# Optimization experiments

Measured on AMD Instinct MI355X. Metric: run time of the kernel, lower is better.

## Reference

```python
import jax, jax.numpy as jnp
import numpy as np

N, E, F_DIM = 30000, 480000, 256
CLS_HID, NUM_CLASS, GEN_HID, MI_HID, BATCH = 128, 16, 64, 128, 4096
COM_L1, COM_L2, LAM, ALPHA, TAU, EPS = 0.5, 0.5, 0.5, 1.0, 0.5, 1e-8


def _glorot(key, shape):
    scale = jnp.sqrt(2.0 / (shape[0] + shape[-1]))
    return scale * jax.random.normal(key, shape, dtype=jnp.float32)


def setup_inputs() -> dict:
    key = jax.random.key(0)
    ks = jax.random.split(key, 32)
    inp = {
        'feat': jax.random.normal(ks[0], (N, F_DIM), dtype=jnp.float32),
        'view1_indices': jax.random.randint(ks[1], (2, E), 0, N),
        'view1_values': jax.random.uniform(ks[2], (E,), dtype=jnp.float32),
        'view2_indices': jax.random.randint(ks[3], (2, E), 0, N),
        'view2_values': jax.random.uniform(ks[4], (E,), dtype=jnp.float32),
        'idx': jnp.sort(jax.random.randint(ks[5], (BATCH,), 0, N)),
        # GenView (v1 and v2): gen_gcn weight + gen_mlp (Linear(2*gen_hid, 1))
        'W_gen_v1': _glorot(ks[6], (F_DIM, GEN_HID)),
        'Wm_v1': _glorot(ks[7], (2 * GEN_HID, 1)),
        'bm_v1': jnp.zeros((1,), dtype=jnp.float32),
        'W_gen_v2': _glorot(ks[8], (F_DIM, GEN_HID)),
        'Wm_v2': _glorot(ks[9], (2 * GEN_HID, 1)),
        'bm_v2': jnp.zeros((1,), dtype=jnp.float32),
        # Classification: three two-layer GCN encoders (v1, v2, v)
        'W1_v1': _glorot(ks[10], (F_DIM, CLS_HID)), 'W2_v1': _glorot(ks[11], (CLS_HID, NUM_CLASS)),
        'W1_v2': _glorot(ks[12], (F_DIM, CLS_HID)), 'W2_v2': _glorot(ks[13], (CLS_HID, NUM_CLASS)),
        'W1_v': _glorot(ks[14], (F_DIM, CLS_HID)), 'W2_v': _glorot(ks[15], (CLS_HID, NUM_CLASS)),
        # MI_NCE: three single GCN layers + shared projection MLP
        'Wg': _glorot(ks[16], (F_DIM, MI_HID)),
        'Wg1': _glorot(ks[17], (F_DIM, MI_HID)),
        'Wg2': _glorot(ks[18], (F_DIM, MI_HID)),
        'Wp1': _glorot(ks[19], (MI_HID, MI_HID)), 'bp1': jnp.zeros((MI_HID,), dtype=jnp.float32),
        'Wp2': _glorot(ks[20], (MI_HID, MI_HID)), 'bp2': jnp.zeros((MI_HID,), dtype=jnp.float32),
    }
    return inp


def spmm(idx, vals, x, n):
    # sparse COO adj (idx [2,E], vals [E]) @ dense x [n,d]
    return jax.ops.segment_sum(vals[:, None] * x[idx[1]], idx[0], num_segments=n)


def gcn_layer(x, idx, vals, W, n, act):
    h = spmm(idx, vals, x @ W, n)
    return jax.nn.relu(h) if act else h


def two_layer(x, idx, vals, W1, W2, n):
    return gcn_layer(gcn_layer(x, idx, vals, W1, n, True), idx, vals, W2, n, False)


def sparse_row_softmax(scores, rows, n):
    m = jax.lax.stop_gradient(jax.ops.segment_max(scores, rows, num_segments=n))
    e = jnp.exp(scores - m[rows])
    s = jax.ops.segment_sum(e, rows, num_segments=n)
    return e / s[rows]


def gen_view(feat, idx, vals, Wg, Wm, bm, com_lambda, n):
    emb = gcn_layer(feat, idx, vals, Wg, n, True)
    ff = jnp.concatenate([emb[idx[0]], emb[idx[1]]], axis=-1)  # [E, 2*gen_hid]
    temp = (ff @ Wm + bm).reshape(-1)
    pi = sparse_row_softmax(temp, idx[0], n)  # torch.sparse.softmax(dim=1)
    return vals + com_lambda * pi  # same sparsity pattern as v_ori


def sym(idx, vals):
    # normalize1 (big=True): adj + adj.T as COO concat (duplicates sum in spmm)
    return jnp.concatenate([idx, idx[::-1]], axis=1), jnp.concatenate([vals, vals])


def get_weight(prob):
    top2 = jax.lax.top_k(prob, 2)[0]
    fir, sec = top2[:, 0], top2[:, 1]
    return jnp.exp(ALPHA * (LAM * jnp.log(fir + EPS) + (1.0 - LAM) * jnp.log(fir - sec + EPS)))


def contrast_cal(z1, z2):
    num = z1 @ z2.T
    den = jnp.linalg.norm(z1, axis=-1, keepdims=True) @ jnp.linalg.norm(z2, axis=-1, keepdims=True).T
    m12 = jnp.exp(num / den / TAU)
    m21 = m12.T
    l12 = -jnp.log(jnp.diag(m12 / (m12.sum(1, keepdims=True) + EPS)) + EPS).mean()
    l21 = -jnp.log(jnp.diag(m21 / (m21.sum(1, keepdims=True) + EPS)) + EPS).mean()
    return 0.5 * (l12 + l21)


def cogsl_forward(feat, view1_values, view2_values,
                  W_gen_v1, Wm_v1, bm_v1, W_gen_v2, Wm_v2, bm_v2,
                  W1_v1, W2_v1, W1_v2, W2_v2, W1_v, W2_v,
                  Wg, Wg1, Wg2, Wp1, bp1, Wp2, bp2,
                  view1_indices, view2_indices, idx):
    n = feat.shape[0]
    # View_Estimator (GenView + normalize1)
    nv1 = gen_view(feat, view1_indices, view1_values, W_gen_v1, Wm_v1, bm_v1, COM_L1, n)
    nv2 = gen_view(feat, view2_indices, view2_values, W_gen_v2, Wm_v2, bm_v2, COM_L2, n)
    i1, v1 = sym(view1_indices, nv1)
    i2, v2 = sym(view2_indices, nv2)
    # Classification on each generated view
    prob_v1 = jax.nn.softmax(two_layer(feat, i1, v1, W1_v1, W2_v1, n), axis=1)
    prob_v2 = jax.nn.softmax(two_layer(feat, i2, v2, W1_v2, W2_v2, n), axis=1)
    logits_v1 = jnp.log(prob_v1 + EPS)
    logits_v2 = jnp.log(prob_v2 + EPS)
    # Fusion: per-node convex combination of the two sparse views (row scaling)
    w1 = get_weight(prob_v1)
    w2 = get_weight(prob_v2)
    b1 = w1 / (w1 + w2)
    b2 = w2 / (w1 + w2)
    idx_f = jnp.concatenate([i1, i2], axis=1)
    vals_f = jnp.concatenate([b1[i1[0]] * v1, b2[i2[0]] * v2])
    prob_v = jax.nn.softmax(two_layer(feat, idx_f, vals_f, W1_v, W2_v, n), axis=1)
    logits_v = jnp.log(prob_v + EPS)
    # MI_NCE over [fused v, v1, v2], big=True -> sample `batch` nodes
    proj = lambda h: jax.nn.elu(h @ Wp1 + bp1) @ Wp2 + bp2
    ev = proj(gcn_layer(feat, idx_f, vals_f, Wg, n, True))[idx]
    e1 = proj(gcn_layer(feat, i1, v1, Wg1, n, True))[idx]
    e2 = proj(gcn_layer(feat, i2, v2, Wg2, n, True))[idx]
    vv1 = contrast_cal(ev, e1)
    vv2 = contrast_cal(ev, e2)
    v1v2 = contrast_cal(e1, e2)
    return jnp.concatenate([logits_v.ravel(), logits_v1.ravel(), logits_v2.ravel(),
                            jnp.stack([vv1, vv2, v1v2])])


def reference(feat, view1_indices, view1_values, view2_indices, view2_values, idx,
              W_gen_v1, Wm_v1, bm_v1, W_gen_v2, Wm_v2, bm_v2,
              W1_v1, W2_v1, W1_v2, W2_v2, W1_v, W2_v,
              Wg, Wg1, Wg2, Wp1, bp1, Wp2, bp2):
    return cogsl_forward(feat, view1_values, view2_values,
                         W_gen_v1, Wm_v1, bm_v1, W_gen_v2, Wm_v2, bm_v2,
                         W1_v1, W2_v1, W1_v2, W2_v2, W1_v, W2_v,
                         Wg, Wg1, Wg2, Wp1, bp1, Wp2, bp2,
                         view1_indices, view2_indices, idx)
```

## Files before the change

### kernel.cpp

```cpp
#include <hip/hip_runtime.h>
#include <math.h>

#define NN 30000
#define EE 480000
#define FD 256
#define CH 128
#define NCLS 16
#define GH 64
#define MH 128
#define BT 4096
#define EPSc 1e-8f
#define GBc ((NN + 127) / 128)
#define SPB8 ((NN + 7) / 8)
#define SPB16 ((NN + 15) / 16)
#define RBc ((BT + 15) / 16)
#define NOX (SPB16 + 3 * RBc)

typedef __attribute__((ext_vector_type(8))) short short8;
typedef __attribute__((ext_vector_type(4))) float f32x4;

__device__ __forceinline__ unsigned short f2bf(float x) {
    unsigned b = __float_as_uint(x);
    unsigned r = b + 0x7FFFu + ((b >> 16) & 1u);
    return (unsigned short)(r >> 16);
}
__device__ __forceinline__ float bf2f(unsigned short h) {
    return __uint_as_float(((unsigned)h) << 16);
}
__device__ __forceinline__ float4 fma4(float s, float4 x, float4 a) {
    a.x = fmaf(s, x.x, a.x); a.y = fmaf(s, x.y, a.y);
    a.z = fmaf(s, x.z, a.z); a.w = fmaf(s, x.w, a.w);
    return a;
}

__global__ void split_bf16(const float* __restrict__ x, unsigned short* __restrict__ hi,
                           unsigned short* __restrict__ lo, long n) {
    long i = (long)blockIdx.x * 256 + threadIdx.x;
    if (i >= n) return;
    float v = x[i];
    unsigned short h = f2bf(v);
    hi[i] = h;
    lo[i] = f2bf(v - bf2f(h));
}

struct WSArgs {
    const float* s[8];
    unsigned short* h[8];
    unsigned short* l[8];
};
__global__ void wsplit_all(WSArgs a) {
    constexpr int NNp[8] = {64, 64, 128, 128, 128, 128, 128, 128};
    constexpr int OFF[9] = {0, 16384, 32768, 65536, 98304, 131072, 163840, 196608, 229376};
    int i = blockIdx.x * 256 + threadIdx.x;
    if (i >= 229376) return;
    int w = 0;
#pragma unroll
    for (int t = 1; t < 8; t++) if (i >= OFF[t]) w = t;
    int j = i - OFF[w];
    int N = NNp[w];
    int k = j / N, n = j % N;
    float v = a.s[w][j];
    unsigned short hh = f2bf(v);
    a.h[w][(size_t)n * 256 + k] = hh;
    a.l[w][(size_t)n * 256 + k] = f2bf(v - bf2f(hh));
}

template <int NT, bool OUT16>
__device__ __forceinline__ void gemm3_body(
    unsigned short* sm, int bx,
    const unsigned short* __restrict__ Ahi, const unsigned short* __restrict__ Alo,
    const unsigned short* __restrict__ BThi, const unsigned short* __restrict__ BTlo,
    int K, void* __restrict__ Cv, int Cstride, int M)
{
    unsigned short* Ah = sm;
    unsigned short* Al = Ah + 128 * 40;
    unsigned short* Bh = Al + 128 * 40;
    unsigned short* Bl = Bh + NT * 16 * 40;
    int t = threadIdx.x;
    int w = t >> 6, l = t & 63;
    int lane = l & 15, quad = l >> 4;
    int row0 = bx * 128;
    f32x4 acc[2][NT];
#pragma unroll
    for (int s = 0; s < 2; s++)
#pragma unroll
        for (int n = 0; n < NT; n++) acc[s][n] = (f32x4)(0.f);

    int ar = t >> 1, ako = (t & 1) << 4;
    int nkc = K >> 5;
    for (int kc = 0; kc < nkc; kc++) {
        int kb = kc << 5;
        {
            int gr = row0 + ar;
            float4 h0, h1, l0, l1;
            if (gr < M) {
                const float4* pH = (const float4*)&Ahi[(size_t)gr * K + kb + ako];
                const float4* pL = (const float4*)&Alo[(size_t)gr * K + kb + ako];
                h0 = pH[0]; h1 = pH[1]; l0 = pL[0]; l1 = pL[1];
            } else {
                h0 = h1 = l0 = l1 = make_float4(0.f, 0.f, 0.f, 0.f);
            }
            float4* dH = (float4*)&Ah[ar * 40 + ako];
            dH[0] = h0; dH[1] = h1;
            float4* dL = (float4*)&Al[ar * 40 + ako];
            dL[0] = l0; dL[1] = l1;
        }
        if (ar < NT * 16) {
            const float4* pH = (const float4*)&BThi[(size_t)ar * K + kb + ako];
            const float4* pL = (const float4*)&BTlo[(size_t)ar * K + kb + ako];
            float4 h0 = pH[0], h1 = pH[1], l0 = pL[0], l1 = pL[1];
            float4* dH = (float4*)&Bh[ar * 40 + ako];
            dH[0] = h0; dH[1] = h1;
            float4* dL = (float4*)&Bl[ar * 40 + ako];
            dL[0] = l0; dL[1] = l1;
        }
        __syncthreads();
        short8 aH[2], aL[2];
// ... 58 lines not shown
    int nkc = K >> 5;
    for (int kc = 0; kc < nkc; kc++) {
        int kb = kc << 5;
        {
            int gr = row0 + ar;
            float4 h0, h1;
            if (gr < M) {
                const float4* pH = (const float4*)&Ahi[(size_t)gr * K + kb + ako];
                h0 = pH[0]; h1 = pH[1];
            } else {
                h0 = h1 = make_float4(0.f, 0.f, 0.f, 0.f);
            }
            float4* dH = (float4*)&Ah[ar * 40 + ako];
            dH[0] = h0; dH[1] = h1;
        }
        if (ar < NT * 16) {
            const float4* pH = (const float4*)&BThi[(size_t)ar * K + kb + ako];
            float4 h0 = pH[0], h1 = pH[1];
            float4* dH = (float4*)&Bh[ar * 40 + ako];
            dH[0] = h0; dH[1] = h1;
        }
        __syncthreads();
        short8 aH[2];
#pragma unroll
        for (int s = 0; s < 2; s++)
            aH[s] = *(const short8*)&Ah[(w * 32 + s * 16 + lane) * 40 + quad * 8];
#pragma unroll
        for (int n = 0; n < NT; n++) {
            short8 bH = *(const short8*)&Bh[(n * 16 + lane) * 40 + quad * 8];
#pragma unroll
            for (int s = 0; s < 2; s++)
                acc[s][n] = __builtin_amdgcn_mfma_f32_16x16x32_bf16(aH[s], bH, acc[s][n], 0, 0, 0);
        }
        __syncthreads();
    }
#pragma unroll
    for (int s = 0; s < 2; s++) {
        int rb = row0 + w * 32 + s * 16 + quad * 4;
#pragma unroll
        for (int reg = 0; reg < 4; reg++) {
            int gr = rb + reg;
            if (gr >= M) continue;
#pragma unroll
            for (int n = 0; n < NT; n++) {
                if (OUT16)
                    ((unsigned short*)Cv)[(size_t)gr * Cstride + n * 16 + lane] = f2bf(acc[s][n][reg]);
                else
                    ((float*)Cv)[(size_t)gr * Cstride + n * 16 + lane] = acc[s][n][reg];
            }
        }
    }
}

__global__ __launch_bounds__(256) void mega0(
    const int* __restrict__ i1, const int* __restrict__ i2, int* __restrict__ cnt,
    int* __restrict__ sd1, int* __restrict__ sd2,
    int* __restrict__ sc1, int* __restrict__ sc2,
    const unsigned short* __restrict__ feat_hi,
    const unsigned short* __restrict__ w1vh, unsigned short* __restrict__ Ph2,
    const unsigned short* __restrict__ wgallh, unsigned short* __restrict__ Pmi16)
{
    __shared__ unsigned short sm[128 * 40 + 8 * 16 * 40];
    int b = blockIdx.x;
    if (b < GBc) {
        gemm1_body<8, true>(sm, b, feat_hi, w1vh, FD, Ph2, 128, NN);
        return;
    }
    b -= GBc;
    if (b < 3 * GBc) {
        int y = b / GBc, bx = b % GBc;
        gemm1_body<8, true>(sm, bx, feat_hi, wgallh + (size_t)y * 32768,
                            FD, Pmi16 + (size_t)y * 128, 384, NN);
        return;
    }
    b -= 3 * GBc;
    int e = b * 256 + threadIdx.x;
    if (e >= EE) return;
    int r1 = i1[e], c1 = i1[EE + e];
    int r2 = i2[e], c2 = i2[EE + e];
    sd1[e] = atomicAdd(&cnt[r1], 1);
    sd2[e] = atomicAdd(&cnt[NN + r2], 1);
    sc1[e] = atomicAdd(&cnt[2 * NN + c1], 1);
    sc2[e] = atomicAdd(&cnt[3 * NN + c2], 1);
}

__global__ __launch_bounds__(256) void mega1(
    const int* __restrict__ i1, const float* __restrict__ v1,
    const int* __restrict__ i2, const float* __restrict__ v2,
    const int* __restrict__ sd1, const int* __restrict__ sd2,
    const int* __restrict__ sc1, const int* __restrict__ sc2,
    const int* __restrict__ rp4,
    int2* __restrict__ ed1, int2* __restrict__ ec1,
    int2* __restrict__ ed2, int2* __restrict__ ec2,
    const unsigned short* __restrict__ feat_hi, const unsigned short* __restrict__ feat_lo,
    const unsigned short* __restrict__ wgen12h, const unsigned short* __restrict__ wgen12l,
    float* __restrict__ Pg,
    const unsigned short* __restrict__ w1pairh, const unsigned short* __restrict__ w1pairl,
    float* __restrict__ P01)
{
    __shared__ unsigned short sm[128 * 40 * 2 + 8 * 16 * 40 * 2];
    int b = blockIdx.x;
    if (b < GBc) {
        gemm3_body<8, false>(sm, b, feat_hi, feat_lo, wgen12h, wgen12l, FD, Pg, 128, NN);
        return;
    }
    b -= GBc;
    if (b < 2 * GBc) {
        int y = b / GBc, bx = b % GBc;
        gemm3_body<8, false>(sm, bx, feat_hi, feat_lo,
                             w1pairh + (size_t)y * 32768, w1pairl + (size_t)y * 32768,
                             FD, P01 + (size_t)y * 128, 256, NN);
        return;
    }
    b -= 2 * GBc;
    int e = b * 256 + threadIdx.x;
    if (e >= EE) return;
    const int* rp_d1 = rp4;
    const int* rp_d2 = rp4 + (NN + 1);
    const int* rp_c1 = rp4 + 2 * (NN + 1);
    const int* rp_c2 = rp4 + 3 * (NN + 1);
    int r = i1[e], c = i1[EE + e];
    int p = rp_d1[r] + sd1[e];
    ed1[p] = make_int2(c, __float_as_int(v1[e]));
    ec1[rp_c1[c] + sc1[e]] = make_int2(r, p);
    r = i2[e]; c = i2[EE + e];
    p = rp_d2[r] + sd2[e];
    ed2[p] = make_int2(c, __float_as_int(v2[e]));
    ec2[rp_c2[c] + sc2[e]] = make_int2(r, p);
}

__global__ __launch_bounds__(256) void contrast_direct(
    const unsigned short* __restrict__ z16, float* __restrict__ stats)
{
    int p = blockIdx.z;
    int pa = (p == 2) ? 1 : 0;
    int pb = (p == 0) ? 1 : 2;
    const unsigned short* A = z16 + (size_t)pa * BT * MH;
    const unsigned short* B = z16 + (size_t)pb * BT * MH;
    float* diag = stats + (size_t)p * 3 * BT;
    float* rs = diag + BT;
    float* cs = rs + BT;
    int t = threadIdx.x;
    int w = t >> 6, l = t & 63, m = l & 15, quad = l >> 4;
    int i0 = blockIdx.y * 128, j0 = blockIdx.x * 128;

    short8 afr[2][4];
#pragma unroll
    for (int s = 0; s < 2; s++) {
        const unsigned short* arow = &A[(size_t)(i0 + w * 32 + s * 16 + m) * MH + quad * 8];
#pragma unroll
        for (int kc = 0; kc < 4; kc++)
            afr[s][kc] = *(const short8*)(arow + kc * 32);
    }
    f32x4 acc[2][8];
#pragma unroll
    for (int s = 0; s < 2; s++)
#pragma unroll
        for (int n = 0; n < 8; n++) acc[s][n] = (f32x4)(0.f);

#pragma unroll
    for (int kc = 0; kc < 4; kc++) {
#pragma unroll
        for (int n = 0; n < 8; n++) {
            short8 bf = *(const short8*)&B[(size_t)(j0 + n * 16 + m) * MH + kc * 32 + quad * 8];
            acc[0][n] = __builtin_amdgcn_mfma_f32_16x16x32_bf16(afr[0][kc], bf, acc[0][n], 0, 0, 0);
            acc[1][n] = __builtin_amdgcn_mfma_f32_16x16x32_bf16(afr[1][kc], bf, acc[1][n], 0, 0, 0);
        }
// ... 192 lines not shown
    const int* rp = rp_d + y * (NN + 1);
    const int2* arr = y ? e2 : e1;
    int row = blockIdx.x * 16 + threadIdx.x / 16;
    int o = threadIdx.x % 16;
    if (row >= NN) return;
    float4 a[4] = {};
    gath_dir_f32<32>(rp, arr, row, (const float4*)Pg, y * 16 + o, a);
    float4 r;
    r.x = fmaxf((a[0].x + a[1].x) + (a[2].x + a[3].x), 0.f);
    r.y = fmaxf((a[0].y + a[1].y) + (a[2].y + a[3].y), 0.f);
    r.z = fmaxf((a[0].z + a[1].z) + (a[2].z + a[3].z), 0.f);
    r.w = fmaxf((a[0].w + a[1].w) + (a[2].w + a[3].w), 0.f);
    const float* Wmh = (y ? Wm2 : Wm1) + GH;
    float part = r.x * Wmh[o * 4] + r.y * Wmh[o * 4 + 1]
               + r.z * Wmh[o * 4 + 2] + r.w * Wmh[o * 4 + 3];
    part += __shfl_xor(part, 1); part += __shfl_xor(part, 2);
    part += __shfl_xor(part, 4); part += __shfl_xor(part, 8);
    if (o == 0) sb[y * NN + row] = part;
}

__device__ __forceinline__ void softmax16_epi(
    float4 r, int node, float* __restrict__ logits, float* __restrict__ wout)
{
    int o = threadIdx.x & 3;
    float mx = fmaxf(fmaxf(r.x, r.y), fmaxf(r.z, r.w));
    mx = fmaxf(mx, __shfl_xor(mx, 1));
    mx = fmaxf(mx, __shfl_xor(mx, 2));
    float e0 = expf(r.x - mx), e1 = expf(r.y - mx), e2 = expf(r.z - mx), e3 = expf(r.w - mx);
    float s = (e0 + e1) + (e2 + e3);
    s += __shfl_xor(s, 1);
    s += __shfl_xor(s, 2);
    float inv = 1.f / s;
    float p0 = e0 * inv, p1 = e1 * inv, p2 = e2 * inv, p3 = e3 * inv;
    float4 lg;
    lg.x = logf(p0 + EPSc); lg.y = logf(p1 + EPSc);
    lg.z = logf(p2 + EPSc); lg.w = logf(p3 + EPSc);
    ((float4*)logits)[(size_t)node * 4 + o] = lg;
    if (wout) {
        float f = p0, se = -1.f;
        if (p1 > f) { se = f; f = p1; } else se = p1;
        if (p2 > f) { se = f; f = p2; } else if (p2 > se) se = p2;
        if (p3 > f) { se = f; f = p3; } else if (p3 > se) se = p3;
#pragma unroll
        for (int d = 1; d <= 2; d <<= 1) {
            float of = __shfl_xor(f, d), os = __shfl_xor(se, d);
            if (of > f) { se = fmaxf(f, os); f = of; }
            else se = fmaxf(se, of);
        }
        if (o == 0)
            wout[node] = expf(0.5f * logf(f + EPSc) + 0.5f * logf(f - se + EPSc));
    }
}

__global__ __launch_bounds__(256) void spmm16_softmax_pair(
    const int* __restrict__ rp_d, const int* __restrict__ rp_c,
    const int2* __restrict__ ed1, const int2* __restrict__ ec1, const float* __restrict__ nvd1,
    const int2* __restrict__ ed2, const int2* __restrict__ ec2, const float* __restrict__ nvd2,
    const float* __restrict__ R01, float* __restrict__ logits_base, float* __restrict__ w12)
{
    int y = blockIdx.y;
    const int* rpd = rp_d + y * (NN + 1);
    const int* rpc = rp_c + y * (NN + 1);
    const int2* ed = y ? ed2 : ed1;
    const int2* ec = y ? ec2 : ec1;
    const float* nvd = y ? nvd2 : nvd1;
    int row = blockIdx.x * 64 + threadIdx.x / 4;
    int o = threadIdx.x % 4;
    if (row >= NN) return;
    const float4* x4 = (const float4*)(R01 + (size_t)y * NN * 16);
    float4 a[4] = {};
    gath_dir_f32<4>(rpd, ed, row, x4, o, a);
    gath_csc_f32<4>(rpc, ec, nvd, row, x4, o, a);
    float4 r;
    r.x = (a[0].x + a[1].x) + (a[2].x + a[3].x);
    r.y = (a[0].y + a[1].y) + (a[2].y + a[3].y);
    r.z = (a[0].z + a[1].z) + (a[2].z + a[3].z);
    r.w = (a[0].w + a[1].w) + (a[2].w + a[3].w);
    softmax16_epi(r, row, logits_base + (size_t)y * NN * NCLS, w12 + (size_t)y * NN);
}

__global__ __launch_bounds__(256) void spmm16_fused_softmax(
    const int* __restrict__ rp_d, const int* __restrict__ rp_c,
    const int2* __restrict__ ed1, const int2* __restrict__ ec1, const float* __restrict__ nvd1,
    const int2* __restrict__ ed2, const int2* __restrict__ ec2, const float* __restrict__ nvd2,
    const float* __restrict__ w12, const float* __restrict__ x, float* __restrict__ logits)
{
    int row = blockIdx.x * 64 + threadIdx.x / 4;
    int o = threadIdx.x % 4;
    if (row >= NN) return;
    const float4* x4 = (const float4*)x;
    float4 a[4] = {};
    gath_dir_f32<4>(rp_d, ed1, row, x4, o, a);
    gath_csc_f32<4>(rp_c, ec1, nvd1, row, x4, o, a);
    float4 s1;
    s1.x = (a[0].x + a[1].x) + (a[2].x + a[3].x);
    s1.y = (a[0].y + a[1].y) + (a[2].y + a[3].y);
    s1.z = (a[0].z + a[1].z) + (a[2].z + a[3].z);
    s1.w = (a[0].w + a[1].w) + (a[2].w + a[3].w);
    float4 b[4] = {};
    gath_dir_f32<4>(rp_d + (NN + 1), ed2, row, x4, o, b);
    gath_csc_f32<4>(rp_c + (NN + 1), ec2, nvd2, row, x4, o, b);
    float4 s2;
    s2.x = (b[0].x + b[1].x) + (b[2].x + b[3].x);
    s2.y = (b[0].y + b[1].y) + (b[2].y + b[3].y);
    s2.z = (b[0].z + b[1].z) + (b[2].z + b[3].z);
    s2.w = (b[0].w + b[1].w) + (b[2].w + b[3].w);
    float wa = w12[row], wb = w12[NN + row];
    float inv = 1.f / (wa + wb);
    float w1 = wa * inv, w2 = wb * inv;
    float4 r;
    r.x = w1 * s1.x + w2 * s2.x;
    r.y = w1 * s1.y + w2 * s2.y;
    r.z = w1 * s1.z + w2 * s2.z;
    r.w = w1 * s1.w + w2 * s2.w;
    softmax16_epi(r, row, logits, nullptr);
}

__device__ __forceinline__ void gath_dir_b16(
    const int* __restrict__ rp, const int2* __restrict__ ed, int row,
    const unsigned short* __restrict__ X, int xstride, int o, float* acc)
{
    int p0 = rp[row], p1 = rp[row + 1];
    int j = p0;
    for (; j + 8 <= p1; j += 8) {
        int2 q[8]; short8 x[8];
#pragma unroll
        for (int e = 0; e < 8; e++) q[e] = ed[j + e];
#pragma unroll
        for (int e = 0; e < 8; e++)
            x[e] = *(const short8*)&X[(size_t)q[e].x * xstride + o * 8];
#pragma unroll
        for (int e = 0; e < 8; e++) {
            float v = __int_as_float(q[e].y);
#pragma unroll
            for (int k = 0; k < 8; k++)
                acc[k] = fmaf(v, bf2f((unsigned short)x[e][k]), acc[k]);
        }
    }
    for (; j + 4 <= p1; j += 4) {
        int2 q0 = ed[j], q1 = ed[j+1], q2 = ed[j+2], q3 = ed[j+3];
// ... 130 lines not shown
    int row = bx * 16 + r;
    if (row >= NN) return;
    float a1[8] = {}, a2[8] = {};
    gath_dir_b16(rp_d, ed1, row, Ph2, 128, o, a1);
    gath_csc_b16(rp_c, ec1, nvd1, row, Ph2, 128, o, a1);
    gath_dir_b16(rp_d + (NN + 1), ed2, row, Ph2, 128, o, a2);
    gath_csc_b16(rp_c + (NN + 1), ec2, nvd2, row, Ph2, 128, o, a2);
    float* o1 = A1 + (size_t)row * 128 + o * 8;
    float* o2 = A2 + (size_t)row * 128 + o * 8;
    *(float4*)&o1[0] = make_float4(a1[0], a1[1], a1[2], a1[3]);
    *(float4*)&o1[4] = make_float4(a1[4], a1[5], a1[6], a1[7]);
    *(float4*)&o2[0] = make_float4(a2[0], a2[1], a2[2], a2[3]);
    *(float4*)&o2[4] = make_float4(a2[4], a2[5], a2[6], a2[7]);
}

__device__ __forceinline__ void spmm128f_body(
    float* sm, int bx, int y, const int* __restrict__ rp_d, const int* __restrict__ rp_c,
    const int2* __restrict__ ed, const int2* __restrict__ ec, const float* __restrict__ nvd,
    const float* __restrict__ P01, const float* __restrict__ W2, float* __restrict__ R01)
{
    float* W2s = sm;
    float* Qs  = sm + 2048;
    for (int i = threadIdx.x; i < 2048; i += 256) W2s[i] = W2[i];
    int r = threadIdx.x / 32;
    int o = threadIdx.x % 32;
    int row = bx * 8 + r;
    float4 a[4] = {};
    if (row < NN) {
        gath_dir_f32<64>(rp_d + y * (NN + 1), ed, row, (const float4*)P01, y * 32 + o, a);
        gath_csc_f32<64>(rp_c + y * (NN + 1), ec, nvd, row, (const float4*)P01, y * 32 + o, a);
    }
    float4 q;
    q.x = fmaxf((a[0].x + a[1].x) + (a[2].x + a[3].x), 0.f);
    q.y = fmaxf((a[0].y + a[1].y) + (a[2].y + a[3].y), 0.f);
    q.z = fmaxf((a[0].z + a[1].z) + (a[2].z + a[3].z), 0.f);
    q.w = fmaxf((a[0].w + a[1].w) + (a[2].w + a[3].w), 0.f);
    *(float4*)&Qs[r * 128 + o * 4] = q;
    __syncthreads();
    int t = threadIdx.x;
    if (t < 128) {
        int rr = t >> 4, c = t & 15;
        int grow = bx * 8 + rr;
        if (grow < NN) {
            float acc = 0.f;
            const float* qrow = &Qs[rr * 128];
#pragma unroll 8
            for (int k = 0; k < 128; k++)
                acc = fmaf(qrow[k], W2s[k * 16 + c], acc);
            R01[((size_t)y * NN + grow) * 16 + c] = acc;
        }
    }
}

__global__ __launch_bounds__(256) void mega23(
    const int* __restrict__ rp_d, const int* __restrict__ rp_c,
    const int2* __restrict__ ed1, const int2* __restrict__ ec1, const float* __restrict__ nvd1,
    const int2* __restrict__ ed2, const int2* __restrict__ ec2, const float* __restrict__ nvd2,
    const float* __restrict__ P01, const float* __restrict__ W2v1, const float* __restrict__ W2v2,
    float* __restrict__ R01,
    const int* __restrict__ rows, const unsigned short* __restrict__ Pmi,
    float* __restrict__ zQ,
    const unsigned short* __restrict__ Ph2,
    float* __restrict__ A1, float* __restrict__ A2,
    float* __restrict__ G1, float* __restrict__ G2)
{
    __shared__ float sm[2048 + 8 * 128];
    int b = blockIdx.x;
    int u = b >> 2, r = b & 3;
    if (r == 3) {
        if (u < SPB16) {
            b2gather_body(u, rp_d, rp_c, ed1, ec1, nvd1, ed2, ec2, nvd2, Ph2, A1, A2);
            return;
        }
        u -= SPB16;
        if (u < 2 * RBc) {
            int y = 1 + u / RBc;
            rows_b16_body(u % RBc, y, rp_d, rp_c, ed1, ec1, nvd1, ed2, ec2, nvd2,
                          rows, Pmi, zQ);
            return;
        }
        u -= 2 * RBc;
        rows0_gather_body(u, rp_d, rp_c, ed1, ec1, nvd1, ed2, ec2, nvd2,
                          rows, Pmi, G1, G2);
        return;
    }
    int s = u * 3 + r;
    if (s >= 2 * SPB8) return;
    int y = s / SPB8;
    spmm128f_body(sm, s % SPB8, y, rp_d, rp_c, y ? ed2 : ed1, y ? ec2 : ec1,
                  y ? nvd2 : nvd1, P01, y ? W2v2 : W2v1, R01);
}

__global__ __launch_bounds__(256) void combineB2(
    const float* __restrict__ w12,
    const float* __restrict__ A1, const float* __restrict__ A2,
    const float* __restrict__ W2v, float* __restrict__ R2,
    const int* __restrict__ rows,
    const float* __restrict__ G1, const float* __restrict__ G2,
    float* __restrict__ zQ)
{
    __shared__ float sm[2048 + 16 * 128];
    int b = blockIdx.x;
    int r = threadIdx.x / 16;
    int o = threadIdx.x % 16;
    if (b < SPB16) {
        float* W2s = sm;
        float* Qs  = sm + 2048;
        for (int i = threadIdx.x; i < 2048; i += 256) W2s[i] = W2v[i];
        int row = b * 16 + r;
        float wa = w12[row], wb = w12[NN + row];
        float inv = 1.f / (wa + wb);
        float w1 = wa * inv, w2 = wb * inv;
        const float* p1 = A1 + (size_t)row * 128 + o * 8;
        const float* p2 = A2 + (size_t)row * 128 + o * 8;
#pragma unroll
        for (int k = 0; k < 8; k++)
            Qs[r * 128 + o * 8 + k] = fmaxf(w1 * p1[k] + w2 * p2[k], 0.f);
        __syncthreads();
        int t = threadIdx.x;
        int rr = t >> 4, c = t & 15;
        int grow = b * 16 + rr;
        float acc = 0.f;
        const float* qrow = &Qs[rr * 128];
#pragma unroll 8
        for (int k = 0; k < 128; k++)
            acc = fmaf(qrow[k], W2s[k * 16 + c], acc);
        R2[(size_t)grow * 16 + c] = acc;
        return;
    }
    b -= SPB16;
    int ri = b * 16 + r;
    if (ri >= BT) return;
    int node = rows[ri];
    float wa = w12[node], wb = w12[NN + node];
    float inv = 1.f / (wa + wb);
    float w1 = wa * inv, w2 = wb * inv;
    const float* p1 = G1 + (size_t)ri * 128 + o * 8;
    const float* p2 = G2 + (size_t)ri * 128 + o * 8;
    float* out = zQ + (size_t)ri * 128 + o * 8;
#pragma unroll
    for (int k = 0; k < 8; k++)
        out[k] = fmaxf(w1 * p1[k] + w2 * p2[k], 0.f);
}

__global__ __launch_bounds__(256) void proj_norm8(
    const float* __restrict__ zQ,
    const float* __restrict__ Wp1, const float* __restrict__ bp1,
    const float* __restrict__ Wp2, const float* __restrict__ bp2,
    unsigned short* __restrict__ z16)
{
    __shared__ float g[8 * MH], u[8 * MH];
    __shared__ float red[4][4];
    int t = threadIdx.x;
    size_t base = (size_t)blockIdx.y * BT + (size_t)blockIdx.x * 8;
    for (int idx = t; idx < 8 * MH; idx += 256)
        g[idx] = zQ[(base + (idx >> 7)) * MH + (idx & 127)];
    __syncthreads();
    int col = t & 127;
    int rh = t >> 7;
    float acc[4];
    float b1 = bp1[col];
#pragma unroll
    for (int rr = 0; rr < 4; rr++) acc[rr] = b1;
    for (int k = 0; k < MH; k++) {
        float wk = Wp1[k * MH + col];
#pragma unroll
        for (int rr = 0; rr < 4; rr++)
            acc[rr] = fmaf(g[(rh * 4 + rr) * MH + k], wk, acc[rr]);
    }
#pragma unroll
    for (int rr = 0; rr < 4; rr++)
        u[(rh * 4 + rr) * MH + col] = acc[rr] > 0.f ? acc[rr] : (expf(acc[rr]) - 1.f);
    __syncthreads();
    float z[4];
    float b2 = bp2[col];
#pragma unroll
    for (int rr = 0; rr < 4; rr++) z[rr] = b2;
    for (int k = 0; k < MH; k++) {
        float wk = Wp2[k * MH + col];
#pragma unroll
        for (int rr = 0; rr < 4; rr++)
            z[rr] = fmaf(u[(rh * 4 + rr) * MH + k], wk, z[rr]);
    }
    float sq[4];
#pragma unroll
    for (int rr = 0; rr < 4; rr++) sq[rr] = z[rr] * z[rr];
#pragma unroll
    for (int off = 32; off; off >>= 1) {
#pragma unroll
        for (int rr = 0; rr < 4; rr++) sq[rr] += __shfl_xor(sq[rr], off);
    }
    int w = t >> 6;
    if ((t & 63) == 0) {
#pragma unroll
        for (int rr = 0; rr < 4; rr++) red[w][rr] = sq[rr];
    }
    __syncthreads();
#pragma unroll
    for (int rr = 0; rr < 4; rr++) {
        float nrm = sqrtf(red[rh * 2][rr] + red[rh * 2 + 1][rr]);
        z16[(base + rh * 4 + rr) * MH + col] = f2bf(z[rr] / nrm);
    }
}

__global__ void contrast_reduce(const float* __restrict__ stats, float* __restrict__ out3)
{
    int p = blockIdx.x, t = threadIdx.x;
    const float* diag = stats + (size_t)p * 3 * BT;
    const float* rs = diag + BT;
    const float* cs = rs + BT;
    float s1 = 0.f, s2 = 0.f;
    for (int i = t; i < BT; i += 256) {
        float d = diag[i];
        s1 += logf(d / (rs[i] + EPSc) + EPSc);
        s2 += logf(d / (cs[i] + EPSc) + EPSc);
    }
#pragma unroll
    for (int off = 32; off; off >>= 1) { s1 += __shfl_down(s1, off); s2 += __shfl_down(s2, off); }
    __shared__ float sh[8];
    if ((t & 63) == 0) { sh[(t >> 6) * 2] = s1; sh[(t >> 6) * 2 + 1] = s2; }
    __syncthreads();
    if (t == 0) {
        float a = sh[0] + sh[2] + sh[4] + sh[6];
        float b = sh[1] + sh[3] + sh[5] + sh[7];
        out3[p] = 0.5f * (-a / BT - b / BT);
    }
}

extern "C" void kernel_launch(void* const* d_in, const int* in_sizes, int n_in,
                              void* d_out, int out_size, void* d_ws, size_t ws_size,
                              hipStream_t stream)
{
    const float* feat   = (const float*)d_in[0];
    const int*   ind1   = (const int*)d_in[1];
    const float* vals1  = (const float*)d_in[2];
    const int*   ind2   = (const int*)d_in[3];
    const float* vals2  = (const float*)d_in[4];
    const int*   idxb   = (const int*)d_in[5];
    const float* Wm1    = (const float*)d_in[7];
    const float* Wm2    = (const float*)d_in[10];
    const float* W2_v1  = (const float*)d_in[13];
    const float* W2_v2  = (const float*)d_in[15];
    const float* W2_v   = (const float*)d_in[17];
    const float* Wp1    = (const float*)d_in[21];
    const float* bp1    = (const float*)d_in[22];
    const float* Wp2    = (const float*)d_in[23];
    const float* bp2    = (const float*)d_in[24];
    float* dout = (float*)d_out;

    float* ws = (float*)d_ws;
    size_t off = 0;
    auto alloc = [&](size_t n) { n = (n + 3) & ~(size_t)3; float* p = ws + off; off += n; return p; };
    auto alloc_s = [&](size_t n) { return (unsigned short*)alloc((n + 1) / 2); };

    float* pool = alloc(16000000);
    float* Pg   = pool;
    float* P01  = pool + 3840000;
    float* R01  = pool + 11520000;
    float* zQ   = pool + 12480000;
    float* A1   = pool;
    float* G1   = pool + 14052864;
    float* G2   = pool + 14577152;
    float* R2   = pool + 15101440;

    unsigned short* feat_hi = alloc_s((size_t)NN * FD);
    unsigned short* feat_lo = alloc_s((size_t)NN * FD);
    float* A2 = (float*)feat_hi;
    unsigned short* Ph2d    = alloc_s((size_t)NN * CH);
    unsigned short* Pmi16d  = alloc_s((size_t)NN * 384);
    float* sb   = alloc(2 * NN);
    float* w12  = alloc(2 * NN);
    float* stats = alloc((size_t)3 * 3 * BT);
    unsigned short* z16 = alloc_s((size_t)3 * BT * MH);
    int2* ed1 = (int2*)alloc(2 * (size_t)EE);
    int2* ed2 = (int2*)alloc(2 * (size_t)EE);
    int2* ec1 = (int2*)alloc(2 * (size_t)EE);
    int2* ec2 = (int2*)alloc(2 * (size_t)EE);
    float* nvd1 = alloc(EE);
    float* nvd2 = alloc(EE);
    int* sd1 = (int*)alloc(EE);
    int* sd2 = (int*)alloc(EE);
    int* sc1 = (int*)alloc(EE);
    int* sc2 = (int*)alloc(EE);
    int* rp4  = (int*)alloc(4 * (NN + 1));
    int* cnt4 = (int*)alloc(4 * NN);
    int* bsum = (int*)alloc(128);
    int* rp_d = rp4;
    int* rp_c = rp4 + 2 * (NN + 1);
    unsigned short* wgen12h = alloc_s(32768); unsigned short* wgen12l = alloc_s(32768);
    unsigned short* w1pairh = alloc_s(65536); unsigned short* w1pairl = alloc_s(65536);
    unsigned short* w1vh    = alloc_s(32768); unsigned short* w1vl    = alloc_s(32768);
    unsigned short* wgallh  = alloc_s(98304); unsigned short* wgalll  = alloc_s(98304);

    const int NB = (NN + 1 + 1023) / 1024;
    const int NCNT = (EE + 255) / 256;

    hipMemsetAsync(cnt4, 0, 4 * NN * 4, stream);
    split_bf16<<<((long)NN * FD + 255) / 256, 256, 0, stream>>>(feat, feat_hi, feat_lo, (long)NN * FD);
    {
        WSArgs a;
        a.s[0] = (const float*)d_in[6];  a.h[0] = wgen12h;          a.l[0] = wgen12l;
        a.s[1] = (const float*)d_in[9];  a.h[1] = wgen12h + 16384;  a.l[1] = wgen12l + 16384;
        a.s[2] = (const float*)d_in[12]; a.h[2] = w1pairh;          a.l[2] = w1pairl;
        a.s[3] = (const float*)d_in[14]; a.h[3] = w1pairh + 32768;  a.l[3] = w1pairl + 32768;
        a.s[4] = (const float*)d_in[16]; a.h[4] = w1vh;             a.l[4] = w1vl;
        a.s[5] = (const float*)d_in[18]; a.h[5] = wgallh;           a.l[5] = wgalll;
        a.s[6] = (const float*)d_in[19]; a.h[6] = wgallh + 32768;   a.l[6] = wgalll + 32768;
        a.s[7] = (const float*)d_in[20]; a.h[7] = wgallh + 65536;   a.l[7] = wgalll + 65536;
        wsplit_all<<<(229376 + 255) / 256, 256, 0, stream>>>(a);
    }

    mega0<<<4 * GBc + NCNT, 256, 0, stream>>>(ind1, ind2, cnt4, sd1, sd2, sc1, sc2,
                                              feat_hi, w1vh, Ph2d, wgallh, Pmi16d);

    scan_block4<<<dim3(NB, 4), 1024, 0, stream>>>(cnt4, rp4, bsum);
    scan_bsum4<<<4, 64, 0, stream>>>(bsum, NB);
    scan_add4<<<dim3(NB, 4), 1024, 0, stream>>>(bsum, rp4);

    mega1<<<3 * GBc + NCNT, 256, 0, stream>>>(ind1, vals1, ind2, vals2,
                                              sd1, sd2, sc1, sc2, rp4,
                                              ed1, ec1, ed2, ec2,
                                              feat_hi, feat_lo, wgen12h, wgen12l, Pg,
                                              w1pairh, w1pairl, P01);

    spmm64_scores<<<dim3((NN + 15) / 16, 2), 256, 0, stream>>>(rp_d, ed1, ed2, Pg, Wm1, Wm2, sb);
    gen_nv<<<dim3((NN + 255) / 256, 2), 256, 0, stream>>>(rp_d, ed1, ed2, sb, nvd1, nvd2);

    mega23<<<4 * NOX, 256, 0, stream>>>(rp_d, rp_c, ed1, ec1, nvd1,
                                        ed2, ec2, nvd2, P01, W2_v1, W2_v2,
                                        R01, idxb, Pmi16d, zQ,
                                        Ph2d, A1, A2, G1, G2);

    spmm16_softmax_pair<<<dim3((NN + 63) / 64, 2), 256, 0, stream>>>(
        rp_d, rp_c, ed1, ec1, nvd1, ed2, ec2, nvd2, R01, dout + (size_t)NN * NCLS, w12);

    combineB2<<<SPB16 + RBc, 256, 0, stream>>>(w12, A1, A2, W2_v, R2, idxb, G1, G2, zQ);

    spmm16_fused_softmax<<<(NN + 63) / 64, 256, 0, stream>>>(
        rp_d, rp_c, ed1, ec1, nvd1, ed2, ec2, nvd2, w12, R2, dout);

    proj_norm8<<<dim3(BT / 8, 3), 256, 0, stream>>>(zQ, Wp1, bp1, Wp2, bp2, z16);
    hipMemsetAsync(stats, 0, (size_t)3 * 3 * BT * 4, stream);
    contrast_direct<<<dim3(32, 32, 3), 256, 0, stream>>>(z16, stats);
    contrast_reduce<<<3, 256, 0, stream>>>(stats, dout + (size_t)3 * NN * NCLS);
}
```

Baseline: 883.3 us.

## Regroup kernel launches into fewer mega-kernels by dependency stage

Merges the feature split, weight split and edge counting into one prep kernel, and moves the bf16 GEMMs for Ph2 and Pmi into mega1x. The old mega23 is split so spmm128f and the rows_b16 gathers run first (mega2). The pair softmax then runs alongside the b2/rows0 gathers and the projection of planes 1 and 2 (pairX), and the plane-0 projection runs alongside the fused softmax (fusedX). The aim is to cut launch count and idle tails by overlapping independent work in each launch, at the cost of more heterogeneous blocks and possible imbalance, such as the GEMMs now sharing a launch with scatter work.

```diff
diff --git a/kernel.cpp b/kernel.cpp
--- a/kernel.cpp
+++ b/kernel.cpp
@@ -14,7 +14,9 @@
 #define SPB8 ((NN + 7) / 8)
 #define SPB16 ((NN + 15) / 16)
 #define RBc ((BT + 15) / 16)
-#define NOX (SPB16 + 3 * RBc)
+#define PRB ((NN + 63) / 64)
+#define PJB (BT / 8)
+#define PX4 1056
 
 typedef __attribute__((ext_vector_type(8))) short short8;
 typedef __attribute__((ext_vector_type(4))) float f32x4;
@@ -31,16 +33,6 @@
     a.x = fmaf(s, x.x, a.x); a.y = fmaf(s, x.y, a.y);
     a.z = fmaf(s, x.z, a.z); a.w = fmaf(s, x.w, a.w);
     return a;
-}
-
-__global__ void split_bf16(const float* __restrict__ x, unsigned short* __restrict__ hi,
-                           unsigned short* __restrict__ lo, long n) {
-    long i = (long)blockIdx.x * 256 + threadIdx.x;
-    if (i >= n) return;
-    float v = x[i];
-    unsigned short h = f2bf(v);
-    hi[i] = h;
-    lo[i] = f2bf(v - bf2f(h));
 }
 
 struct WSArgs {
@@ -48,21 +40,50 @@
     unsigned short* h[8];
     unsigned short* l[8];
 };
-__global__ void wsplit_all(WSArgs a) {
-    constexpr int NNp[8] = {64, 64, 128, 128, 128, 128, 128, 128};
-    constexpr int OFF[9] = {0, 16384, 32768, 65536, 98304, 131072, 163840, 196608, 229376};
-    int i = blockIdx.x * 256 + threadIdx.x;
-    if (i >= 229376) return;
-    int w = 0;
-#pragma unroll
-    for (int t = 1; t < 8; t++) if (i >= OFF[t]) w = t;
-    int j = i - OFF[w];
-    int N = NNp[w];
-    int k = j / N, n = j % N;
-    float v = a.s[w][j];
-    unsigned short hh = f2bf(v);
-    a.h[w][(size_t)n * 256 + k] = hh;
-    a.l[w][(size_t)n * 256 + k] = f2bf(v - bf2f(hh));
+
+__global__ __launch_bounds__(256) void prep_all(
+    const float* __restrict__ feat, unsigned short* __restrict__ fhi,
+    unsigned short* __restrict__ flo, WSArgs a,
+    const int* __restrict__ i1, const int* __restrict__ i2, int* __restrict__ cnt,
+    int* __restrict__ sd1, int* __restrict__ sd2,
+    int* __restrict__ sc1, int* __restrict__ sc2)
+{
+    int b = blockIdx.x;
+    if (b < 30000) {
+        long i = (long)b * 256 + threadIdx.x;
+        float v = feat[i];
+        unsigned short h = f2bf(v);
+        fhi[i] = h;
+        flo[i] = f2bf(v - bf2f(h));
+        return;
+    }
+    b -= 30000;
+    if (b < 896) {
+        int i = b * 256 + threadIdx.x;
+        if (i >= 229376) return;
+        constexpr int NNp[8] = {64, 64, 128, 128, 128, 128, 128, 128};
+        constexpr int OFF[9] = {0, 16384, 32768, 65536, 98304, 131072, 163840, 196608, 229376};
+        int w = 0;
+#pragma unroll
+        for (int t = 1; t < 8; t++) if (i >= OFF[t]) w = t;
+        int j = i - OFF[w];
+        int N = NNp[w];
+        int k = j / N, n = j % N;
+        float v = a.s[w][j];
+        unsigned short hh = f2bf(v);
+        a.h[w][(size_t)n * 256 + k] = hh;
+        a.l[w][(size_t)n * 256 + k] = f2bf(v - bf2f(hh));
+        return;
+    }
+    b -= 896;
+    int e = b * 256 + threadIdx.x;
+    if (e >= EE) return;
+    int r1 = i1[e], c1 = i1[EE + e];
+    int r2 = i2[e], c2 = i2[EE + e];
+    sd1[e] = atomicAdd(&cnt[r1], 1);
+    sd2[e] = atomicAdd(&cnt[NN + r2], 1);
+    sc1[e] = atomicAdd(&cnt[2 * NN + c1], 1);
+    sc2[e] = atomicAdd(&cnt[3 * NN + c2], 1);
 }
 
 template <int NT, bool OUT16>
@@ -227,39 +248,7 @@
     }
 }
 
-__global__ __launch_bounds__(256) void mega0(
-    const int* __restrict__ i1, const int* __restrict__ i2, int* __restrict__ cnt,
-    int* __restrict__ sd1, int* __restrict__ sd2,
-    int* __restrict__ sc1, int* __restrict__ sc2,
-    const unsigned short* __restrict__ feat_hi,
-    const unsigned short* __restrict__ w1vh, unsigned short* __restrict__ Ph2,
-    const unsigned short* __restrict__ wgallh, unsigned short* __restrict__ Pmi16)
-{
-    __shared__ unsigned short sm[128 * 40 + 8 * 16 * 40];
-    int b = blockIdx.x;
-    if (b < GBc) {
-        gemm1_body<8, true>(sm, b, feat_hi, w1vh, FD, Ph2, 128, NN);
-        return;
-    }
-    b -= GBc;
-    if (b < 3 * GBc) {
-        int y = b / GBc, bx = b % GBc;
-        gemm1_body<8, true>(sm, bx, feat_hi, wgallh + (size_t)y * 32768,
-                            FD, Pmi16 + (size_t)y * 128, 384, NN);
-        return;
-    }
-    b -= 3 * GBc;
-    int e = b * 256 + threadIdx.x;
-    if (e >= EE) return;
-    int r1 = i1[e], c1 = i1[EE + e];
-    int r2 = i2[e], c2 = i2[EE + e];
-    sd1[e] = atomicAdd(&cnt[r1], 1);
-    sd2[e] = atomicAdd(&cnt[NN + r2], 1);
-    sc1[e] = atomicAdd(&cnt[2 * NN + c1], 1);
-    sc2[e] = atomicAdd(&cnt[3 * NN + c2], 1);
-}
-
-__global__ __launch_bounds__(256) void mega1(
+__global__ __launch_bounds__(256) void mega1x(
     const int* __restrict__ i1, const float* __restrict__ v1,
     const int* __restrict__ i2, const float* __restrict__ v2,
     const int* __restrict__ sd1, const int* __restrict__ sd2,
@@ -271,7 +260,9 @@
     const unsigned short* __restrict__ wgen12h, const unsigned short* __restrict__ wgen12l,
     float* __restrict__ Pg,
     const unsigned short* __restrict__ w1pairh, const unsigned short* __restrict__ w1pairl,
-    float* __restrict__ P01)
+    float* __restrict__ P01,
+    const unsigned short* __restrict__ w1vh, unsigned short* __restrict__ Ph2,
+    const unsigned short* __restrict__ wgallh, unsigned short* __restrict__ Pmi16)
 {
     __shared__ unsigned short sm[128 * 40 * 2 + 8 * 16 * 40 * 2];
     int b = blockIdx.x;
@@ -288,6 +279,18 @@
         return;
     }
     b -= 2 * GBc;
+    if (b < GBc) {
+        gemm1_body<8, true>(sm, b, feat_hi, w1vh, FD, Ph2, 128, NN);
+        return;
+    }
+    b -= GBc;
+    if (b < 3 * GBc) {
+        int y = b / GBc, bx = b % GBc;
+        gemm1_body<8, true>(sm, bx, feat_hi, wgallh + (size_t)y * 32768,
+                            FD, Pmi16 + (size_t)y * 128, 384, NN);
+        return;
+    }
+    b -= 3 * GBc;
     int e = b * 256 + threadIdx.x;
     if (e >= EE) return;
     const int* rp_d1 = rp4;
@@ -586,19 +589,18 @@
     }
 }
 
-__global__ __launch_bounds__(256) void spmm16_softmax_pair(
-    const int* __restrict__ rp_d, const int* __restrict__ rp_c,
+__device__ __forceinline__ void pair_body(
+    int y, int bx, const int* __restrict__ rp_d, const int* __restrict__ rp_c,
     const int2* __restrict__ ed1, const int2* __restrict__ ec1, const float* __restrict__ nvd1,
     const int2* __restrict__ ed2, const int2* __restrict__ ec2, const float* __restrict__ nvd2,
     const float* __restrict__ R01, float* __restrict__ logits_base, float* __restrict__ w12)
 {
-    int y = blockIdx.y;
     const int* rpd = rp_d + y * (NN + 1);
     const int* rpc = rp_c + y * (NN + 1);
     const int2* ed = y ? ed2 : ed1;
     const int2* ec = y ? ec2 : ec1;
     const float* nvd = y ? nvd2 : nvd1;
-    int row = blockIdx.x * 64 + threadIdx.x / 4;
+    int row = bx * 64 + threadIdx.x / 4;
     int o = threadIdx.x % 4;
     if (row >= NN) return;
     const float4* x4 = (const float4*)(R01 + (size_t)y * NN * 16);
@@ -613,13 +615,13 @@
     softmax16_epi(r, row, logits_base + (size_t)y * NN * NCLS, w12 + (size_t)y * NN);
 }
 
-__global__ __launch_bounds__(256) void spmm16_fused_softmax(
-    const int* __restrict__ rp_d, const int* __restrict__ rp_c,
+__device__ __forceinline__ void fused_body(
+    int bx, const int* __restrict__ rp_d, const int* __restrict__ rp_c,
     const int2* __restrict__ ed1, const int2* __restrict__ ec1, const float* __restrict__ nvd1,
     const int2* __restrict__ ed2, const int2* __restrict__ ec2, const float* __restrict__ nvd2,
     const float* __restrict__ w12, const float* __restrict__ x, float* __restrict__ logits)
 {
-    int row = blockIdx.x * 64 + threadIdx.x / 4;
+    int row = bx * 64 + threadIdx.x / 4;
     int o = threadIdx.x % 4;
     if (row >= NN) return;
     const float4* x4 = (const float4*)x;
@@ -856,43 +858,127 @@
     }
 }
 
-__global__ __launch_bounds__(256) void mega23(
+__global__ __launch_bounds__(256) void mega2(
     const int* __restrict__ rp_d, const int* __restrict__ rp_c,
     const int2* __restrict__ ed1, const int2* __restrict__ ec1, const float* __restrict__ nvd1,
     const int2* __restrict__ ed2, const int2* __restrict__ ec2, const float* __restrict__ nvd2,
     const float* __restrict__ P01, const float* __restrict__ W2v1, const float* __restrict__ W2v2,
     float* __restrict__ R01,
     const int* __restrict__ rows, const unsigned short* __restrict__ Pmi,
-    float* __restrict__ zQ,
-    const unsigned short* __restrict__ Ph2,
-    float* __restrict__ A1, float* __restrict__ A2,
-    float* __restrict__ G1, float* __restrict__ G2)
+    float* __restrict__ zQ)
 {
     __shared__ float sm[2048 + 8 * 128];
     int b = blockIdx.x;
+    if (b < 2 * SPB8) {
+        int y = b / SPB8;
+        spmm128f_body(sm, b % SPB8, y, rp_d, rp_c, y ? ed2 : ed1, y ? ec2 : ec1,
+                      y ? nvd2 : nvd1, P01, y ? W2v2 : W2v1, R01);
+        return;
+    }
+    b -= 2 * SPB8;
+    int y = 1 + b / RBc;
+    rows_b16_body(b % RBc, y, rp_d, rp_c, ed1, ec1, nvd1, ed2, ec2, nvd2,
+                  rows, Pmi, zQ);
+}
+
+__device__ __forceinline__ void proj8_body(
+    float* g, float* u, float* red, int bx, int plane,
+    const float* __restrict__ zQ,
+    const float* __restrict__ Wp1, const float* __restrict__ bp1,
+    const float* __restrict__ Wp2, const float* __restrict__ bp2,
+    unsigned short* __restrict__ z16)
+{
+    int t = threadIdx.x;
+    size_t base = (size_t)plane * BT + (size_t)bx * 8;
+    for (int idx = t; idx < 8 * MH; idx += 256)
+        g[idx] = zQ[(base + (idx >> 7)) * MH + (idx & 127)];
+    __syncthreads();
+    int col = t & 127;
+    int rh = t >> 7;
+    float acc[4];
+    float b1 = bp1[col];
+#pragma unroll
+    for (int rr = 0; rr < 4; rr++) acc[rr] = b1;
+    for (int k = 0; k < MH; k++) {
+        float wk = Wp1[k * MH + col];
+#pragma unroll
+        for (int rr = 0; rr < 4; rr++)
+            acc[rr] = fmaf(g[(rh * 4 + rr) * MH + k], wk, acc[rr]);
+    }
+#pragma unroll
+    for (int rr = 0; rr < 4; rr++)
+        u[(rh * 4 + rr) * MH + col] = acc[rr] > 0.f ? acc[rr] : (expf(acc[rr]) - 1.f);
+    __syncthreads();
+    float z[4];
+    float b2 = bp2[col];
+#pragma unroll
+    for (int rr = 0; rr < 4; rr++) z[rr] = b2;
+    for (int k = 0; k < MH; k++) {
+        float wk = Wp2[k * MH + col];
+#pragma unroll
+        for (int rr = 0; rr < 4; rr++)
+            z[rr] = fmaf(u[(rh * 4 + rr) * MH + k], wk, z[rr]);
+    }
+    float sq[4];
+#pragma unroll
+    for (int rr = 0; rr < 4; rr++) sq[rr] = z[rr] * z[rr];
+#pragma unroll
+    for (int off = 32; off; off >>= 1) {
+#pragma unroll
+        for (int rr = 0; rr < 4; rr++) sq[rr] += __shfl_xor(sq[rr], off);
+    }
+    int w = t >> 6;
+    if ((t & 63) == 0) {
+#pragma unroll
+        for (int rr = 0; rr < 4; rr++) red[w * 4 + rr] = sq[rr];
+    }
+    __syncthreads();
+#pragma unroll
+    for (int rr = 0; rr < 4; rr++) {
+        float nrm = sqrtf(red[(rh * 2) * 4 + rr] + red[(rh * 2 + 1) * 4 + rr]);
+        z16[(base + rh * 4 + rr) * MH + col] = f2bf(z[rr] / nrm);
+    }
+}
+
+__global__ __launch_bounds__(256) void pairX(
+    const int* __restrict__ rp_d, const int* __restrict__ rp_c,
+    const int2* __restrict__ ed1, const int2* __restrict__ ec1, const float* __restrict__ nvd1,
+    const int2* __restrict__ ed2, const int2* __restrict__ ec2, const float* __restrict__ nvd2,
+    const float* __restrict__ R01, float* __restrict__ logits_base, float* __restrict__ w12,
+    const unsigned short* __restrict__ Ph2, float* __restrict__ A1, float* __restrict__ A2,
+    const int* __restrict__ rows, const unsigned short* __restrict__ Pmi,
+    float* __restrict__ G1, float* __restrict__ G2,
+    const float* __restrict__ zQ,
+    const float* __restrict__ Wp1, const float* __restrict__ bp1,
+    const float* __restrict__ Wp2, const float* __restrict__ bp2,
+    unsigned short* __restrict__ z16)
+{
+    __shared__ float psm[2064];
+    int b = blockIdx.x;
     int u = b >> 2, r = b & 3;
-    if (r == 3) {
-        if (u < SPB16) {
-            b2gather_body(u, rp_d, rp_c, ed1, ec1, nvd1, ed2, ec2, nvd2, Ph2, A1, A2);
-            return;
-        }
-        u -= SPB16;
-        if (u < 2 * RBc) {
-            int y = 1 + u / RBc;
-            rows_b16_body(u % RBc, y, rp_d, rp_c, ed1, ec1, nvd1, ed2, ec2, nvd2,
-                          rows, Pmi, zQ);
-            return;
-        }
-        u -= 2 * RBc;
-        rows0_gather_body(u, rp_d, rp_c, ed1, ec1, nvd1, ed2, ec2, nvd2,
+    if (r == 0) {
+        if (u < 2 * PRB)
+            pair_body(u / PRB, u % PRB, rp_d, rp_c, ed1, ec1, nvd1, ed2, ec2, nvd2,
+                      R01, logits_base, w12);
+        return;
+    }
+    int idx = u * 3 + (r - 1);
+    if (idx < SPB16) {
+        b2gather_body(idx, rp_d, rp_c, ed1, ec1, nvd1, ed2, ec2, nvd2, Ph2, A1, A2);
+        return;
+    }
+    idx -= SPB16;
+    if (idx < RBc) {
+        rows0_gather_body(idx, rp_d, rp_c, ed1, ec1, nvd1, ed2, ec2, nvd2,
                           rows, Pmi, G1, G2);
         return;
     }
-    int s = u * 3 + r;
-    if (s >= 2 * SPB8) return;
-    int y = s / SPB8;
-    spmm128f_body(sm, s % SPB8, y, rp_d, rp_c, y ? ed2 : ed1, y ? ec2 : ec1,
-                  y ? nvd2 : nvd1, P01, y ? W2v2 : W2v1, R01);
+    idx -= RBc;
+    if (idx < 2 * PJB) {
+        int plane = 1 + idx / PJB;
+        proj8_body(psm, psm + 1024, psm + 2048, idx % PJB, plane,
+                   zQ, Wp1, bp1, Wp2, bp2, z16);
+    }
 }
 
 __global__ __launch_bounds__(256) void combineB2(
@@ -947,64 +1033,23 @@
         out[k] = fmaxf(w1 * p1[k] + w2 * p2[k], 0.f);
 }
 
-__global__ __launch_bounds__(256) void proj_norm8(
+__global__ __launch_bounds__(256) void fusedX(
+    const int* __restrict__ rp_d, const int* __restrict__ rp_c,
+    const int2* __restrict__ ed1, const int2* __restrict__ ec1, const float* __restrict__ nvd1,
+    const int2* __restrict__ ed2, const int2* __restrict__ ec2, const float* __restrict__ nvd2,
+    const float* __restrict__ w12, const float* __restrict__ R2, float* __restrict__ logits,
     const float* __restrict__ zQ,
     const float* __restrict__ Wp1, const float* __restrict__ bp1,
     const float* __restrict__ Wp2, const float* __restrict__ bp2,
     unsigned short* __restrict__ z16)
 {
-    __shared__ float g[8 * MH], u[8 * MH];
-    __shared__ float red[4][4];
-    int t = threadIdx.x;
-    size_t base = (size_t)blockIdx.y * BT + (size_t)blockIdx.x * 8;
-    for (int idx = t; idx < 8 * MH; idx += 256)
-        g[idx] = zQ[(base + (idx >> 7)) * MH + (idx & 127)];
-    __syncthreads();
-    int col = t & 127;
-    int rh = t >> 7;
-    float acc[4];
-    float b1 = bp1[col];
-#pragma unroll
-    for (int rr = 0; rr < 4; rr++) acc[rr] = b1;
-    for (int k = 0; k < MH; k++) {
-        float wk = Wp1[k * MH + col];
-#pragma unroll
-        for (int rr = 0; rr < 4; rr++)
-            acc[rr] = fmaf(g[(rh * 4 + rr) * MH + k], wk, acc[rr]);
-    }
-#pragma unroll
-    for (int rr = 0; rr < 4; rr++)
-        u[(rh * 4 + rr) * MH + col] = acc[rr] > 0.f ? acc[rr] : (expf(acc[rr]) - 1.f);
-    __syncthreads();
-    float z[4];
-    float b2 = bp2[col];
-#pragma unroll
-    for (int rr = 0; rr < 4; rr++) z[rr] = b2;
-    for (int k = 0; k < MH; k++) {
-        float wk = Wp2[k * MH + col];
-#pragma unroll
-        for (int rr = 0; rr < 4; rr++)
-            z[rr] = fmaf(u[(rh * 4 + rr) * MH + k], wk, z[rr]);
-    }
-    float sq[4];
-#pragma unroll
-    for (int rr = 0; rr < 4; rr++) sq[rr] = z[rr] * z[rr];
-#pragma unroll
-    for (int off = 32; off; off >>= 1) {
-#pragma unroll
-        for (int rr = 0; rr < 4; rr++) sq[rr] += __shfl_xor(sq[rr], off);
-    }
-    int w = t >> 6;
-    if ((t & 63) == 0) {
-#pragma unroll
-        for (int rr = 0; rr < 4; rr++) red[w][rr] = sq[rr];
-    }
-    __syncthreads();
-#pragma unroll
-    for (int rr = 0; rr < 4; rr++) {
-        float nrm = sqrtf(red[rh * 2][rr] + red[rh * 2 + 1][rr]);
-        z16[(base + rh * 4 + rr) * MH + col] = f2bf(z[rr] / nrm);
-    }
+    __shared__ float psm[2064];
+    int b = blockIdx.x;
+    if (b < PRB) {
+        fused_body(b, rp_d, rp_c, ed1, ec1, nvd1, ed2, ec2, nvd2, w12, R2, logits);
+        return;
+    }
+    proj8_body(psm, psm + 1024, psm + 2048, b - PRB, 0, zQ, Wp1, bp1, Wp2, bp2, z16);
 }
 
 __global__ void contrast_reduce(const float* __restrict__ stats, float* __restrict__ out3)
@@ -1100,51 +1145,47 @@
     const int NCNT = (EE + 255) / 256;
 
     hipMemsetAsync(cnt4, 0, 4 * NN * 4, stream);
-    split_bf16<<<((long)NN * FD + 255) / 256, 256, 0, stream>>>(feat, feat_hi, feat_lo, (long)NN * FD);
-    {
-        WSArgs a;
-        a.s[0] = (const float*)d_in[6];  a.h[0] = wgen12h;          a.l[0] = wgen12l;
-        a.s[1] = (const float*)d_in[9];  a.h[1] = wgen12h + 16384;  a.l[1] = wgen12l + 16384;
-        a.s[2] = (const float*)d_in[12]; a.h[2] = w1pairh;          a.l[2] = w1pairl;
-        a.s[3] = (const float*)d_in[14]; a.h[3] = w1pairh + 32768;  a.l[3] = w1pairl + 32768;
-        a.s[4] = (const float*)d_in[16]; a.h[4] = w1vh;             a.l[4] = w1vl;
-        a.s[5] = (const float*)d_in[18]; a.h[5] = wgallh;           a.l[5] = wgalll;
-        a.s[6] = (const float*)d_in[19]; a.h[6] = wgallh + 32768;   a.l[6] = wgalll + 32768;
-        a.s[7] = (const float*)d_in[20]; a.h[7] = wgallh + 65536;   a.l[7] = wgalll + 65536;
-        wsplit_all<<<(229376 + 255) / 256, 256, 0, stream>>>(a);
-    }
-
-    mega0<<<4 * GBc + NCNT, 256, 0, stream>>>(ind1, ind2, cnt4, sd1, sd2, sc1, sc2,
-                                              feat_hi, w1vh, Ph2d, wgallh, Pmi16d);
+    WSArgs a;
+    a.s[0] = (const float*)d_in[6];  a.h[0] = wgen12h;          a.l[0] = wgen12l;
+    a.s[1] = (const float*)d_in[9];  a.h[1] = wgen12h + 16384;  a.l[1] = wgen12l + 16384;
+    a.s[2] = (const float*)d_in[12]; a.h[2] = w1pairh;          a.l[2] = w1pairl;
+    a.s[3] = (const float*)d_in[14]; a.h[3] = w1pairh + 32768;  a.l[3] = w1pairl + 32768;
+    a.s[4] = (const float*)d_in[16]; a.h[4] = w1vh;             a.l[4] = w1vl;
+    a.s[5] = (const float*)d_in[18]; a.h[5] = wgallh;           a.l[5] = wgalll;
+    a.s[6] = (const float*)d_in[19]; a.h[6] = wgallh + 32768;   a.l[6] = wgalll + 32768;
+    a.s[7] = (const float*)d_in[20]; a.h[7] = wgallh + 65536;   a.l[7] = wgalll + 65536;
+    prep_all<<<30000 + 896 + NCNT, 256, 0, stream>>>(feat, feat_hi, feat_lo, a,
+                                                     ind1, ind2, cnt4, sd1, sd2, sc1, sc2);
 
     scan_block4<<<dim3(NB, 4), 1024, 0, stream>>>(cnt4, rp4, bsum);
     scan_bsum4<<<4, 64, 0, stream>>>(bsum, NB);
     scan_add4<<<dim3(NB, 4), 1024, 0, stream>>>(bsum, rp4);
 
-    mega1<<<3 * GBc + NCNT, 256, 0, stream>>>(ind1, vals1, ind2, vals2,
-                                              sd1, sd2, sc1, sc2, rp4,
-                                              ed1, ec1, ed2, ec2,
-                                              feat_hi, feat_lo, wgen12h, wgen12l, Pg,
-                                              w1pairh, w1pairl, P01);
+    mega1x<<<7 * GBc + NCNT, 256, 0, stream>>>(ind1, vals1, ind2, vals2,
+                                               sd1, sd2, sc1, sc2, rp4,
+                                               ed1, ec1, ed2, ec2,
+                                               feat_hi, feat_lo, wgen12h, wgen12l, Pg,
+                                               w1pairh, w1pairl, P01,
+                                               w1vh, Ph2d, wgallh, Pmi16d);
 
     spmm64_scores<<<dim3((NN + 15) / 16, 2), 256, 0, stream>>>(rp_d, ed1, ed2, Pg, Wm1, Wm2, sb);
     gen_nv<<<dim3((NN + 255) / 256, 2), 256, 0, stream>>>(rp_d, ed1, ed2, sb, nvd1, nvd2);
-
-    mega23<<<4 * NOX, 256, 0, stream>>>(rp_d, rp_c, ed1, ec1, nvd1,
-                                        ed2, ec2, nvd2, P01, W2_v1, W2_v2,
-                                        R01, idxb, Pmi16d, zQ,
-                                        Ph2d, A1, A2, G1, G2);
-
-    spmm16_softmax_pair<<<dim3((NN + 63) / 64, 2), 256, 0, stream>>>(
-        rp_d, rp_c, ed1, ec1, nvd1, ed2, ec2, nvd2, R01, dout + (size_t)NN * NCLS, w12);
+    hipMemsetAsync(stats, 0, (size_t)3 * 3 * BT * 4, stream);
+
+    mega2<<<2 * SPB8 + 2 * RBc, 256, 0, stream>>>(rp_d, rp_c, ed1, ec1, nvd1,
+                                                  ed2, ec2, nvd2, P01, W2_v1, W2_v2,
+                                                  R01, idxb, Pmi16d, zQ);
+
+    pairX<<<4 * PX4, 256, 0, stream>>>(rp_d, rp_c, ed1, ec1, nvd1, ed2, ec2, nvd2,
+                                       R01, dout + (size_t)NN * NCLS, w12,
+                                       Ph2d, A1, A2, idxb, Pmi16d, G1, G2,
+                                       zQ, Wp1, bp1, Wp2, bp2, z16);
 
     combineB2<<<SPB16 + RBc, 256, 0, stream>>>(w12, A1, A2, W2_v, R2, idxb, G1, G2, zQ);
 
-    spmm16_fused_softmax<<<(NN + 63) / 64, 256, 0, stream>>>(
-        rp_d, rp_c, ed1, ec1, nvd1, ed2, ec2, nvd2, w12, R2, dout);
-
-    proj_norm8<<<dim3(BT / 8, 3), 256, 0, stream>>>(zQ, Wp1, bp1, Wp2, bp2, z16);
-    hipMemsetAsync(stats, 0, (size_t)3 * 3 * BT * 4, stream);
+    fusedX<<<PRB + PJB, 256, 0, stream>>>(rp_d, rp_c, ed1, ec1, nvd1, ed2, ec2, nvd2,
+                                          w12, R2, dout, zQ, Wp1, bp1, Wp2, bp2, z16);
+
     contrast_direct<<<dim3(32, 32, 3), 256, 0, stream>>>(z16, stats);
     contrast_reduce<<<3, 256, 0, stream>>>(stats, dout + (size_t)3 * NN * NCLS);
 }
```

Result: faster. 746.1 us (-15.5%).
